# Optimization experiments

Hardware: AMD Instinct MI355X
Metric: run time of the kernel (lower is better)

Reference implementation:

```python
import jax, jax.numpy as jnp
import numpy as np
from jax import lax

B, L, D_MODEL = 4, 512, 256
N_LAYERS = 6
EXPAND = 2
D_INNER = EXPAND * D_MODEL  # 512
D_STATE = 16
D_CONV = 4
DT_RANK = (D_MODEL + 15) // 16  # 16
EPS = 1e-5


def silu(x):
    return x * jax.nn.sigmoid(x)


def rmsnorm(x, w):
    var = jnp.mean(x * x, axis=-1, keepdims=True)
    return x * lax.rsqrt(var + EPS) * w


def setup_inputs() -> dict:
    key = jax.random.key(0)
    ks = jax.random.split(key, 12)
    s = lambda *sh: 0.02
    inp = {
        "x": jax.random.normal(ks[0], (B, L, D_MODEL), dtype=jnp.float32),
        "norm_w": jnp.ones((N_LAYERS, D_MODEL), jnp.float32),
        "W_in": jax.random.normal(ks[1], (N_LAYERS, 2 * D_INNER, D_MODEL), jnp.float32) * 0.02,
        "b_in": jnp.zeros((N_LAYERS, 2 * D_INNER), jnp.float32),
        "conv_w": jax.random.normal(ks[2], (N_LAYERS, D_INNER, D_CONV), jnp.float32) * 0.2,
        "W_x": jax.random.normal(ks[3], (N_LAYERS, DT_RANK + 2 * D_STATE, D_INNER), jnp.float32) * 0.02,
        "dt_w": jax.random.normal(ks[4], (N_LAYERS, D_INNER, DT_RANK), jnp.float32) * 0.1,
        "dt_b": jax.random.uniform(ks[5], (N_LAYERS, D_INNER), jnp.float32, -4.0, -2.0),
        "A_log": jnp.log(jnp.broadcast_to(jnp.arange(1, D_STATE + 1, dtype=jnp.float32), (N_LAYERS, D_INNER, D_STATE))),
        "D": jnp.ones((N_LAYERS, D_INNER), jnp.float32),
        "W_out": jax.random.normal(ks[6], (N_LAYERS, D_MODEL, D_INNER), jnp.float32) * 0.02,
        "b_out": jnp.zeros((N_LAYERS, D_MODEL), jnp.float32),
    }
    return inp


def mamba_block(x, W_in, b_in, conv_w, W_x, dt_w, dt_b, A_log, D, W_out, b_out):
    # input projection -> (B, L, 2*d_inner)
    xz = jnp.einsum("bld,ed->ble", x, W_in) + b_in
    xin, z = xz[..., :D_INNER], xz[..., D_INNER:]
    # depthwise causal conv over time (groups = d_inner, left pad d_conv-1)
    xc = lax.conv_general_dilated(
        xin.transpose(0, 2, 1),            # (B, C, L)
        conv_w[:, None, :],                # (C, 1, K)
        window_strides=(1,),
        padding=[(D_CONV - 1, 0)],
        feature_group_count=D_INNER,
        dimension_numbers=("NCH", "OIH", "NCH"),
    ).transpose(0, 2, 1)
    u = silu(xc)                           # (B, L, d_inner)
    # data-dependent dt, B, C
    xdbc = jnp.einsum("bld,rd->blr", u, W_x)
    dt = xdbc[..., :DT_RANK]
    Bm = xdbc[..., DT_RANK:DT_RANK + D_STATE]
    Cm = xdbc[..., DT_RANK + D_STATE:]
    delta = jax.nn.softplus(jnp.einsum("blr,dr->bld", dt, dt_w) + dt_b)
    A = -jnp.exp(A_log)                    # (d_inner, d_state)
    dA = jnp.exp(jnp.einsum("bld,dn->bldn", delta, A))
    dBu = jnp.einsum("bld,bln->bldn", delta * u, Bm)
    # selective scan over time
    def step(h, inp):
        dA_t, dBu_t, C_t = inp
        h = dA_t * h + dBu_t               # (B, d_inner, d_state)
        y_t = jnp.einsum("bdn,bn->bd", h, C_t)
        return h, y_t
    h0 = jnp.zeros((B, D_INNER, D_STATE), x.dtype)
    _, ys = lax.scan(step, h0, (dA.transpose(1, 0, 2, 3), dBu.transpose(1, 0, 2, 3), Cm.transpose(1, 0, 2)))
    y = ys.transpose(1, 0, 2) + u * D      # skip connection D*u
    y = y * silu(z)
    return jnp.einsum("bld,md->blm", y, W_out) + b_out


def reference(x, norm_w, W_in, b_in, conv_w, W_x, dt_w, dt_b, A_log, D, W_out, b_out):
    for i in range(N_LAYERS):
        x = x + mamba_block(rmsnorm(x, norm_w[i]), W_in[i], b_in[i], conv_w[i], W_x[i], dt_w[i], dt_b[i], A_log[i], D[i], W_out[i], b_out[i])
    return x
```

## Files before the change

### kernel.cpp

```cpp
#include <hip/hip_runtime.h>
#include <hip/hip_bf16.h>

#define B_SZ 4
#define L_SZ 512
#define D_MODEL 256
#define D_INNER 512
#define D_STATE 16
#define DT_RANK 16
#define N_LAYERS 6
#define BL (B_SZ * L_SZ)

typedef __bf16 bf16_t;
typedef __bf16 bf16x8 __attribute__((ext_vector_type(8)));
typedef __bf16 bf16x4 __attribute__((ext_vector_type(4)));
typedef float  f32x4  __attribute__((ext_vector_type(4)));

__device__ __forceinline__ float row_allreduce16(float x)
{
    int v;
    v = __builtin_amdgcn_mov_dpp(__float_as_int(x), 0x121, 0xf, 0xf, true);
    x += __int_as_float(v);
    v = __builtin_amdgcn_mov_dpp(__float_as_int(x), 0x122, 0xf, 0xf, true);
    x += __int_as_float(v);
    v = __builtin_amdgcn_mov_dpp(__float_as_int(x), 0x124, 0xf, 0xf, true);
    x += __int_as_float(v);
    v = __builtin_amdgcn_mov_dpp(__float_as_int(x), 0x128, 0xf, 0xf, true);
    x += __int_as_float(v);
    return x;
}

__global__ __launch_bounds__(256) void cast3_kernel(
    const float* __restrict__ s0, const float* __restrict__ s1,
    const float* __restrict__ s2, bf16_t* __restrict__ dst,
    int n0, int n1, int n2)
{
    int i = blockIdx.x * 256 + threadIdx.x;
    const float* s; int off;
    if (i < n0)            { s = s0; off = i; }
    else if (i < n0 + n1)  { s = s1; off = i - n0; }
    else if (i < n0+n1+n2) { s = s2; off = i - n0 - n1; }
    else return;
    const float4 v = *(const float4*)(s + (size_t)off * 4);
    bf16x4 o;
    o[0] = (bf16_t)v.x; o[1] = (bf16_t)v.y;
    o[2] = (bf16_t)v.z; o[3] = (bf16_t)v.w;
    *(bf16x4*)(dst + (size_t)i * 4) = o;
}

__global__ __launch_bounds__(256) void rmsnorm_kernel(
    const float* __restrict__ x, const float* __restrict__ w,
    bf16_t* __restrict__ o)
{
    int row  = blockIdx.x * 4 + (threadIdx.x >> 6);
    int lane = threadIdx.x & 63;
    const float4 v = *(const float4*)(x + (size_t)row * D_MODEL + lane * 4);
    float ss = v.x * v.x + v.y * v.y + v.z * v.z + v.w * v.w;
    #pragma unroll
    for (int off = 32; off; off >>= 1) ss += __shfl_xor(ss, off);
    float rs = rsqrtf(ss * (1.f / D_MODEL) + 1e-5f);
    const float4 wv = *(const float4*)(w + lane * 4);
    bf16x4 ov;
    ov[0] = (bf16_t)(v.x * rs * wv.x);
    ov[1] = (bf16_t)(v.y * rs * wv.y);
    ov[2] = (bf16_t)(v.z * rs * wv.z);
    ov[3] = (bf16_t)(v.w * rs * wv.w);
    *(bf16x4*)(o + (size_t)row * D_MODEL + lane * 4) = ov;
}

__global__ __launch_bounds__(256) void win_kernel(
    const bf16_t* __restrict__ A,
    const bf16_t* __restrict__ Bw,
    const float* __restrict__ bias,
    float* __restrict__ C,
    float* __restrict__ Z)
{
    constexpr int K = 256, BK = 64;
    __shared__ bf16_t As[64][K + 8];
    __shared__ bf16_t Bs[64][BK + 8];

    const int tid  = threadIdx.x;
    const int wave = tid >> 6, lane = tid & 63;
    const int wm = wave >> 1, wn = wave & 1;
    const int lm = lane & 15, quad = lane >> 4;
    const int m0 = blockIdx.y * 64, n0 = blockIdx.x * 64;

    #pragma unroll
    for (int i = tid; i < 64 * (K / 8); i += 256) {
        int r = i >> 5, c8 = i & 31;
        *(bf16x8*)&As[r][c8 * 8] =
            *(const bf16x8*)(A + (size_t)(m0 + r) * K + c8 * 8);
    }

    f32x4 acc[2][2] = {};
    for (int k0 = 0; k0 < K; k0 += BK) {
        #pragma unroll
        for (int i = tid; i < 64 * (BK / 8); i += 256) {
            int r = i >> 3, c8 = i & 7;
            *(bf16x8*)&Bs[r][c8 * 8] =
                *(const bf16x8*)(Bw + (size_t)(n0 + r) * K + k0 + c8 * 8);
        }
        __syncthreads();
        #pragma unroll
        for (int ks = 0; ks < 2; ++ks) {
            bf16x8 af[2], bfr[2];
            #pragma unroll
            for (int i = 0; i < 2; ++i)
                af[i] = *(const bf16x8*)&As[wm * 32 + i * 16 + lm][k0 + ks * 32 + quad * 8];
            #pragma unroll
            for (int j = 0; j < 2; ++j)
                bfr[j] = *(const bf16x8*)&Bs[wn * 32 + j * 16 + lm][ks * 32 + quad * 8];
            #pragma unroll
            for (int i = 0; i < 2; ++i)
                #pragma unroll
                for (int j = 0; j < 2; ++j)
                    acc[i][j] = __builtin_amdgcn_mfma_f32_16x16x32_bf16(
                        af[i], bfr[j], acc[i][j], 0, 0, 0);
        }
        __syncthreads();
    }

    if (n0 >= D_INNER) {
        #pragma unroll
        for (int i = 0; i < 2; ++i) {
            int rowbase = m0 + wm * 32 + i * 16 + quad * 4;
            #pragma unroll
            for (int j = 0; j < 2; ++j) {
                int col = n0 + wn * 32 + j * 16 + lm;
                float4 o;
                #pragma unroll
                for (int r = 0; r < 4; ++r) {
                    float v = acc[i][j][r] + bias[col];
                    ((float*)&o)[r] = v / (1.f + __expf(-v));
                }
                *(float4*)(Z + (size_t)(col - D_INNER) * BL + rowbase) = o;
            }
        }
        return;
    }

    #pragma unroll
    for (int i = 0; i < 2; ++i) {
        #pragma unroll
        for (int j = 0; j < 2; ++j) {
            int col = n0 + wn * 32 + j * 16 + lm;
            #pragma unroll
            for (int r = 0; r < 4; ++r) {
                int rowm = m0 + wm * 32 + i * 16 + quad * 4 + r;
                C[(size_t)rowm * D_INNER + col] = acc[i][j][r] + bias[col];
            }
        }
    }
}

template<int WM, int WN, int TM_T, int TN_T>
__global__ __launch_bounds__(64 * WM * WN) void gemm_wout(
    const bf16_t* __restrict__ A, int lda,
    const bf16_t* __restrict__ Bw, int ldb,
    const float* __restrict__ bias,
    const float* __restrict__ R, int ldr,
    float* __restrict__ C, int ldc, int K)
{
    constexpr int BK = 64;
    constexpr int BM = WM * TM_T * 16;
    constexpr int BN = WN * TN_T * 16;
    constexpr int NT = 64 * WM * WN;
    constexpr int LDK = BK + 8;
    __shared__ bf16_t As[BM][LDK];
    __shared__ bf16_t Bs[BN][LDK];

    const int tid  = threadIdx.x;
    const int wave = tid >> 6, lane = tid & 63;
    const int wm = wave / WN, wn = wave % WN;
    const int lm = lane & 15, quad = lane >> 4;
    const int m0 = blockIdx.y * BM, n0 = blockIdx.x * BN;

    f32x4 acc[TM_T][TN_T] = {};

    for (int k0 = 0; k0 < K; k0 += BK) {
        #pragma unroll
        for (int i = tid; i < BM * (BK / 8); i += NT) {
            int r = i >> 3, c8 = i & 7;
            *(bf16x8*)&As[r][c8 * 8] =
                *(const bf16x8*)(A + (size_t)(m0 + r) * lda + k0 + c8 * 8);
        }
        #pragma unroll
        for (int i = tid; i < BN * (BK / 8); i += NT) {
            int r = i >> 3, c8 = i & 7;
            *(bf16x8*)&Bs[r][c8 * 8] =
                *(const bf16x8*)(Bw + (size_t)(n0 + r) * ldb + k0 + c8 * 8);
        }
        __syncthreads();
        #pragma unroll
        for (int ks = 0; ks < BK / 32; ++ks) {
            bf16x8 af[TM_T], bfr[TN_T];
            #pragma unroll
            for (int i = 0; i < TM_T; ++i)
                af[i] = *(const bf16x8*)&As[wm * TM_T * 16 + i * 16 + lm][ks * 32 + quad * 8];
            #pragma unroll
            for (int j = 0; j < TN_T; ++j)
                bfr[j] = *(const bf16x8*)&Bs[wn * TN_T * 16 + j * 16 + lm][ks * 32 + quad * 8];
            #pragma unroll
            for (int i = 0; i < TM_T; ++i)
                #pragma unroll
                for (int j = 0; j < TN_T; ++j)
                    acc[i][j] = __builtin_amdgcn_mfma_f32_16x16x32_bf16(
                        af[i], bfr[j], acc[i][j], 0, 0, 0);
        }
        __syncthreads();
    }

    #pragma unroll
    for (int i = 0; i < TM_T; ++i) {
        #pragma unroll
        for (int j = 0; j < TN_T; ++j) {
            int col = n0 + wn * TN_T * 16 + j * 16 + lm;
            #pragma unroll
            for (int r = 0; r < 4; ++r) {
                int rowm = m0 + wm * TM_T * 16 + i * 16 + quad * 4 + r;
                C[(size_t)rowm * ldc + col] =
                    acc[i][j][r] + bias[col] + R[(size_t)rowm * ldr + col];
            }
        }
    }
}

__global__ __launch_bounds__(256) void wx_conv_kernel(
    const float* __restrict__ xzx,
    const float* __restrict__ cw,
    const bf16_t* __restrict__ Bw,
    float* __restrict__ uT,
    float* __restrict__ xdbcT)
{
    constexpr int K = 512;
    __shared__ float  xs[19][516];
    __shared__ bf16_t us[16][520];
    __shared__ f32x4  part[4][3][64];

    const int tid  = threadIdx.x;
    const int wave = tid >> 6, lane = tid & 63;
    const int lm = lane & 15, quad = lane >> 4;
    const int m0 = blockIdx.x * 16;

    for (int q = tid; q < 19 * 128; q += 256) {
        int rx = q >> 7, c4 = (q & 127) * 4;
        int mr = m0 - 3 + rx;
        float4 v = make_float4(0.f, 0.f, 0.f, 0.f);
        if (mr >= 0) v = *(const float4*)(xzx + (size_t)mr * K + c4);
        *(float4*)&xs[rx][c4] = v;
    }
    __syncthreads();

    #pragma unroll
    for (int it = 0; it < 8; ++it) {
        int item = tid + it * 256;
        int d = item >> 2, rg = item & 3;
        const float4 wv = *(const float4*)(cw + d * 4);
        float4 o;
        #pragma unroll
        for (int e = 0; e < 4; ++e) {
            int ro = rg * 4 + e;
            int t  = (m0 + ro) & (L_SZ - 1);
            float a = wv.w * xs[ro + 3][d];
            if (t >= 1) a += wv.z * xs[ro + 2][d];
            if (t >= 2) a += wv.y * xs[ro + 1][d];
            if (t >= 3) a += wv.x * xs[ro + 0][d];
            a = a / (1.f + __expf(-a));
            ((float*)&o)[e] = a;
            us[ro][d] = (bf16_t)a;
        }
        *(float4*)(uT + (size_t)d * BL + m0 + rg * 4) = o;
    }
    __syncthreads();

    f32x4 acc[3] = {};
    const int kb = wave * 128 + quad * 8;
    #pragma unroll
    for (int ks = 0; ks < 4; ++ks) {
        int k0 = kb + ks * 32;
        bf16x8 af = *(const bf16x8*)&us[lm][k0];
        #pragma unroll
        for (int j = 0; j < 3; ++j) {
            bf16x8 bfr = *(const bf16x8*)(Bw + (size_t)(j * 16 + lm) * K + k0);
            acc[j] = __builtin_amdgcn_mfma_f32_16x16x32_bf16(af, bfr, acc[j], 0, 0, 0);
        }
    }
    #pragma unroll
    for (int j = 0; j < 3; ++j) part[wave][j][lane] = acc[j];
    __syncthreads();

    if (tid < 192) {
        int j = tid >> 6, l = tid & 63;
        f32x4 s = part[0][j][l];
        s += part[1][j][l];
        s += part[2][j][l];
        s += part[3][j][l];
        int col = j * 16 + (l & 15);
        float4 v = make_float4(s[0], s[1], s[2], s[3]);
        *(float4*)(xdbcT + (size_t)col * BL + m0 + (l >> 4) * 4) = v;
    }
}

__global__ __launch_bounds__(1024, 8) void scan_kernel(
    const float* __restrict__ xdbcT,
    const float* __restrict__ uT,
    const float* __restrict__ szT,
    const float* __restrict__ dt_w,
    const float* __restrict__ dt_b,
    const float* __restrict__ A_log,
    const float* __restrict__ Dv,
    bf16_t* __restrict__ y)
{
    constexpr int TC = 32;
    constexpr int NW = L_SZ / TC;

    int blk  = blockIdx.x;
    int b    = blk >> 7;
    int dg   = blk & 127;
    int wave = threadIdx.x >> 6;
    int lane = threadIdx.x & 63;
    int d    = dg * 4 + (lane >> 4);
    int n    = lane & 15;

    __shared__ float lds_Ap[NW][64];
    __shared__ float lds_he[NW][64];

    float Adn = -__expf(A_log[d * D_STATE + n]);
    float Dd  = Dv[d];
    int r0 = b * L_SZ + wave * TC;

    const float* Brow = xdbcT  + (size_t)(DT_RANK + n) * BL;
    const float* Crow = xdbcT  + (size_t)(DT_RANK + D_STATE + n) * BL;
    const float* urow = uT     + (size_t)d * BL;
    const float* zrow = szT    + (size_t)d * BL;

    float myd[2];
    {
        float w16[16];
        #pragma unroll
        for (int k4 = 0; k4 < 4; ++k4) {
            float4 wv = *(const float4*)(dt_w + (size_t)d * 16 + k4 * 4);
            w16[k4*4+0] = wv.x; w16[k4*4+1] = wv.y;
            w16[k4*4+2] = wv.z; w16[k4*4+3] = wv.w;
        }
        float bdt = dt_b[d];
        #pragma unroll
        for (int g = 0; g < 2; ++g) {
            int t = r0 + g * 16 + n;
            float a = bdt;
            #pragma unroll
            for (int k = 0; k < 16; ++k)
                a += xdbcT[(size_t)k * BL + t] * w16[k];
            myd[g] = (a > 20.f) ? a : __logf(1.f + __expf(a));
        }
    }
    const int sbase = lane & 48;

    {
        float h = 0.f, P = 1.f;
        #pragma unroll
        for (int g = 0; g < 2; ++g) {
            #pragma unroll
            for (int j4 = 0; j4 < 4; ++j4) {
                int rb = r0 + g * 16 + j4 * 4;
                f32x4 Bv = *(const f32x4*)(Brow + rb);
                f32x4 uv = *(const f32x4*)(urow + rb);
                #pragma unroll
                for (int k = 0; k < 4; ++k) {
                    float dlj = __shfl(myd[g], sbase | (j4 * 4 + k));
                    float dA  = __expf(dlj * Adn);
                    h = dA * h + dlj * uv[k] * Bv[k];
                    P *= dA;
                }
            }
        }
        lds_Ap[wave][lane] = P;
        lds_he[wave][lane] = h;
    }
    __syncthreads();

    float H = 0.f;
    for (int j = 0; j < wave; ++j)
        H = lds_Ap[j][lane] * H + lds_he[j][lane];

    float h = H;
    #pragma unroll
    for (int g = 0; g < 2; ++g) {
        float py[16];
        #pragma unroll
        for (int j4 = 0; j4 < 4; ++j4) {
            int rb = r0 + g * 16 + j4 * 4;
            f32x4 Bv = *(const f32x4*)(Brow + rb);
            f32x4 uv = *(const f32x4*)(urow + rb);
            f32x4 Cc = *(const f32x4*)(Crow + rb);
            #pragma unroll
            for (int k = 0; k < 4; ++k) {
                float dlj = __shfl(myd[g], sbase | (j4 * 4 + k));
                float dA  = __expf(dlj * Adn);
                h = dA * h + dlj * uv[k] * Bv[k];
                py[j4 * 4 + k] = h * Cc[k];
            }
        }
        #pragma unroll
        for (int j = 0; j < 16; ++j)
            py[j] = row_allreduce16(py[j]);
        if (n == 0) {
            #pragma unroll
            for (int j4 = 0; j4 < 4; ++j4) {
                int rb = r0 + g * 16 + j4 * 4;
                f32x4 uv = *(const f32x4*)(urow + rb);
                f32x4 sz = *(const f32x4*)(zrow + rb);
                #pragma unroll
                for (int k = 0; k < 4; ++k) {
                    int row = rb + k;
                    y[(size_t)row * D_INNER + d] =
                        (bf16_t)((py[j4*4+k] + uv[k] * Dd) * sz[k]);
                }
            }
        }
    }
}

extern "C" void kernel_launch(void* const* d_in, const int* in_sizes, int n_in,
                              void* d_out, int out_size, void* d_ws, size_t ws_size,
                              hipStream_t stream)
{
    const float* x_in   = (const float*)d_in[0];
    const float* norm_w = (const float*)d_in[1];
    const float* W_in   = (const float*)d_in[2];
    const float* b_in   = (const float*)d_in[3];
    const float* conv_w = (const float*)d_in[4];
    const float* W_x    = (const float*)d_in[5];
    const float* dt_w   = (const float*)d_in[6];
    const float* dt_b   = (const float*)d_in[7];
    const float* A_log  = (const float*)d_in[8];
    const float* Dv     = (const float*)d_in[9];
    const float* W_out  = (const float*)d_in[10];
    const float* b_out  = (const float*)d_in[11];
    float* out = (float*)d_out;

    float* ws     = (float*)d_ws;
    float* xz     = ws;
    float* uT     = xz     + BL * D_INNER;
    float* szT    = uT     + D_INNER * BL;
    float* xdbcT  = szT    + D_INNER * BL;
    bf16_t* bws   = (bf16_t*)(xdbcT + 48 * BL);
    bf16_t* xn_bf = bws;
    bf16_t* y_bf  = xn_bf + BL * D_MODEL;
    bf16_t* Wi_bf = y_bf  + BL * D_INNER;
    bf16_t* Wx_bf = Wi_bf + N_LAYERS * 2 * D_INNER * D_MODEL;
    bf16_t* Wo_bf = Wx_bf + N_LAYERS * 48 * D_INNER;

    {
        int n0 = N_LAYERS * 2 * D_INNER * D_MODEL / 4;
        int n1 = N_LAYERS * 48 * D_INNER / 4;
        int n2 = N_LAYERS * D_MODEL * D_INNER / 4;
        cast3_kernel<<<(n0 + n1 + n2 + 255) / 256, 256, 0, stream>>>(
            W_in, W_x, W_out, Wi_bf, n0, n1, n2);
    }

    for (int i = 0; i < N_LAYERS; ++i) {
        const float* xcur = (i == 0) ? x_in : out;

        rmsnorm_kernel<<<BL / 4, 256, 0, stream>>>(xcur, norm_w + i * D_MODEL, xn_bf);

        win_kernel<<<dim3(1024 / 64, 2048 / 64), 256, 0, stream>>>(
            xn_bf, Wi_bf + (size_t)i * 2 * D_INNER * D_MODEL,
            b_in + i * 2 * D_INNER, xz, szT);

        wx_conv_kernel<<<BL / 16, 256, 0, stream>>>(
            xz, conv_w + i * D_INNER * 4,
            Wx_bf + (size_t)i * 48 * D_INNER, uT, xdbcT);

        scan_kernel<<<512, 1024, 0, stream>>>(
            xdbcT, uT, szT,
            dt_w + (size_t)i * D_INNER * DT_RANK, dt_b + i * D_INNER,
            A_log + (size_t)i * D_INNER * D_STATE, Dv + i * D_INNER, y_bf);

        gemm_wout<2, 2, 2, 2><<<dim3(256 / 64, 2048 / 64), 256, 0, stream>>>(
            y_bf, D_INNER, Wo_bf + (size_t)i * D_MODEL * D_INNER, D_INNER,
            b_out + i * D_MODEL, xcur, D_MODEL, out, D_MODEL, D_INNER);
    }
}
```

Measured before the change: 537.7 us.

## Compute delta softplus projection in wx_conv kernel and stream it to scan

The dt_w projection and softplus are moved out of the scan kernel into the tail of wx_conv_kernel, which now writes a transposed deltaT buffer. Previously the scan kernel recomputed delta for each of the 16 state lanes of a channel and broadcast it with shuffles. The scan now just loads delta as float4 alongside B and u, removing redundant ALU work and shuffles. The cost is an extra write and read of a BL x D_INNER float buffer through memory, plus an added barrier and loop in wx_conv. The scan's launch bounds hint also drops from 8 to 4.

```diff
diff --git a/kernel.cpp b/kernel.cpp
--- a/kernel.cpp
+++ b/kernel.cpp
@@ -228,13 +228,17 @@
     const float* __restrict__ xzx,
     const float* __restrict__ cw,
     const bf16_t* __restrict__ Bw,
+    const float* __restrict__ dt_w,
+    const float* __restrict__ dt_b,
     float* __restrict__ uT,
-    float* __restrict__ xdbcT)
+    float* __restrict__ xdbcT,
+    float* __restrict__ deltaT)
 {
     constexpr int K = 512;
     __shared__ float  xs[19][516];
     __shared__ bf16_t us[16][520];
     __shared__ f32x4  part[4][3][64];
+    __shared__ float  dtt[16][17];
 
     const int tid  = threadIdx.x;
     const int wave = tid >> 6, lane = tid & 63;
@@ -297,15 +301,43 @@
         int col = j * 16 + (l & 15);
         float4 v = make_float4(s[0], s[1], s[2], s[3]);
         *(float4*)(xdbcT + (size_t)col * BL + m0 + (l >> 4) * 4) = v;
-    }
-}
-
-__global__ __launch_bounds__(1024, 8) void scan_kernel(
+        if (j == 0) {
+            #pragma unroll
+            for (int e = 0; e < 4; ++e)
+                dtt[(l >> 4) * 4 + e][l & 15] = s[e];
+        }
+    }
+    __syncthreads();
+
+    #pragma unroll
+    for (int it = 0; it < 8; ++it) {
+        int item = tid + it * 256;
+        int d = item >> 2, tg = item & 3;
+        const float4 w0 = *(const float4*)(dt_w + (size_t)d * 16 + 0);
+        const float4 w1 = *(const float4*)(dt_w + (size_t)d * 16 + 4);
+        const float4 w2 = *(const float4*)(dt_w + (size_t)d * 16 + 8);
+        const float4 w3 = *(const float4*)(dt_w + (size_t)d * 16 + 12);
+        const float bdt = dt_b[d];
+        float4 o;
+        #pragma unroll
+        for (int e = 0; e < 4; ++e) {
+            int t = tg * 4 + e;
+            float a = bdt;
+            a += dtt[t][0]  * w0.x + dtt[t][1]  * w0.y + dtt[t][2]  * w0.z + dtt[t][3]  * w0.w;
+            a += dtt[t][4]  * w1.x + dtt[t][5]  * w1.y + dtt[t][6]  * w1.z + dtt[t][7]  * w1.w;
+            a += dtt[t][8]  * w2.x + dtt[t][9]  * w2.y + dtt[t][10] * w2.z + dtt[t][11] * w2.w;
+            a += dtt[t][12] * w3.x + dtt[t][13] * w3.y + dtt[t][14] * w3.z + dtt[t][15] * w3.w;
+            ((float*)&o)[e] = (a > 20.f) ? a : __logf(1.f + __expf(a));
+        }
+        *(float4*)(deltaT + (size_t)d * BL + m0 + tg * 4) = o;
+    }
+}
+
+__global__ __launch_bounds__(1024, 4) void scan_kernel(
     const float* __restrict__ xdbcT,
+    const float* __restrict__ deltaT,
     const float* __restrict__ uT,
     const float* __restrict__ szT,
-    const float* __restrict__ dt_w,
-    const float* __restrict__ dt_b,
     const float* __restrict__ A_log,
     const float* __restrict__ Dv,
     bf16_t* __restrict__ y)
@@ -325,52 +357,27 @@
     __shared__ float lds_he[NW][64];
 
     float Adn = -__expf(A_log[d * D_STATE + n]);
-    float Dd  = Dv[d];
     int r0 = b * L_SZ + wave * TC;
 
     const float* Brow = xdbcT  + (size_t)(DT_RANK + n) * BL;
     const float* Crow = xdbcT  + (size_t)(DT_RANK + D_STATE + n) * BL;
+    const float* drow = deltaT + (size_t)d * BL;
     const float* urow = uT     + (size_t)d * BL;
     const float* zrow = szT    + (size_t)d * BL;
 
-    float myd[2];
-    {
-        float w16[16];
-        #pragma unroll
-        for (int k4 = 0; k4 < 4; ++k4) {
-            float4 wv = *(const float4*)(dt_w + (size_t)d * 16 + k4 * 4);
-            w16[k4*4+0] = wv.x; w16[k4*4+1] = wv.y;
-            w16[k4*4+2] = wv.z; w16[k4*4+3] = wv.w;
-        }
-        float bdt = dt_b[d];
-        #pragma unroll
-        for (int g = 0; g < 2; ++g) {
-            int t = r0 + g * 16 + n;
-            float a = bdt;
-            #pragma unroll
-            for (int k = 0; k < 16; ++k)
-                a += xdbcT[(size_t)k * BL + t] * w16[k];
-            myd[g] = (a > 20.f) ? a : __logf(1.f + __expf(a));
-        }
-    }
-    const int sbase = lane & 48;
-
     {
         float h = 0.f, P = 1.f;
         #pragma unroll
-        for (int g = 0; g < 2; ++g) {
-            #pragma unroll
-            for (int j4 = 0; j4 < 4; ++j4) {
-                int rb = r0 + g * 16 + j4 * 4;
-                f32x4 Bv = *(const f32x4*)(Brow + rb);
-                f32x4 uv = *(const f32x4*)(urow + rb);
-                #pragma unroll
-                for (int k = 0; k < 4; ++k) {
-                    float dlj = __shfl(myd[g], sbase | (j4 * 4 + k));
-                    float dA  = __expf(dlj * Adn);
-                    h = dA * h + dlj * uv[k] * Bv[k];
-                    P *= dA;
-                }
+        for (int j4 = 0; j4 < 8; ++j4) {
+            int rb = r0 + j4 * 4;
+            f32x4 dl = *(const f32x4*)(drow + rb);
+            f32x4 Bv = *(const f32x4*)(Brow + rb);
+            f32x4 uv = *(const f32x4*)(urow + rb);
+            #pragma unroll
+            for (int k = 0; k < 4; ++k) {
+                float dA = __expf(dl[k] * Adn);
+                h = dA * h + dl[k] * uv[k] * Bv[k];
+                P *= dA;
             }
         }
         lds_Ap[wave][lane] = P;
@@ -382,6 +389,7 @@
     for (int j = 0; j < wave; ++j)
         H = lds_Ap[j][lane] * H + lds_he[j][lane];
 
+    float Dd = Dv[d];
     float h = H;
     #pragma unroll
     for (int g = 0; g < 2; ++g) {
@@ -389,14 +397,14 @@
         #pragma unroll
         for (int j4 = 0; j4 < 4; ++j4) {
             int rb = r0 + g * 16 + j4 * 4;
+            f32x4 dl = *(const f32x4*)(drow + rb);
             f32x4 Bv = *(const f32x4*)(Brow + rb);
             f32x4 uv = *(const f32x4*)(urow + rb);
             f32x4 Cc = *(const f32x4*)(Crow + rb);
             #pragma unroll
             for (int k = 0; k < 4; ++k) {
-                float dlj = __shfl(myd[g], sbase | (j4 * 4 + k));
-                float dA  = __expf(dlj * Adn);
-                h = dA * h + dlj * uv[k] * Bv[k];
+                float dA = __expf(dl[k] * Adn);
+                h = dA * h + dl[k] * uv[k] * Bv[k];
                 py[j4 * 4 + k] = h * Cc[k];
             }
         }
@@ -443,7 +451,8 @@
     float* uT     = xz     + BL * D_INNER;
     float* szT    = uT     + D_INNER * BL;
     float* xdbcT  = szT    + D_INNER * BL;
-    bf16_t* bws   = (bf16_t*)(xdbcT + 48 * BL);
+    float* deltaT = xdbcT  + 48 * BL;
+    bf16_t* bws   = (bf16_t*)(deltaT + D_INNER * BL);
     bf16_t* xn_bf = bws;
     bf16_t* y_bf  = xn_bf + BL * D_MODEL;
     bf16_t* Wi_bf = y_bf  + BL * D_INNER;
@@ -469,11 +478,12 @@
 
         wx_conv_kernel<<<BL / 16, 256, 0, stream>>>(
             xz, conv_w + i * D_INNER * 4,
-            Wx_bf + (size_t)i * 48 * D_INNER, uT, xdbcT);
+            Wx_bf + (size_t)i * 48 * D_INNER,
+            dt_w + (size_t)i * D_INNER * DT_RANK, dt_b + i * D_INNER,
+            uT, xdbcT, deltaT);
 
         scan_kernel<<<512, 1024, 0, stream>>>(
-            xdbcT, uT, szT,
-            dt_w + (size_t)i * D_INNER * DT_RANK, dt_b + i * D_INNER,
+            xdbcT, deltaT, uT, szT,
             A_log + (size_t)i * D_INNER * D_STATE, Dv + i * D_INNER, y_bf);
 
         gemm_wout<2, 2, 2, 2><<<dim3(256 / 64, 2048 / 64), 256, 0, stream>>>(
```

Result: slower. 558.3 us (+3.8%).
